# Kernel tuning notes

Hardware: AMD Instinct MI355X
Metric: run time of the kernel (lower is better)

## Reference

```python
import jax, jax.numpy as jnp
import numpy as np

EPS = 1e-5

def s_block(x, W, g, b, rm, rv):
    # Linear(no bias) -> BatchNorm1d (eval, running stats) -> 1 + tanh
    y = x @ W.T
    y = (y - rm) * jax.lax.rsqrt(rv + EPS) * g + b
    return 1.0 + jnp.tanh(y)

def si_block(x, cw, cb):
    # channel max/mean pool -> concat -> Conv2d(2,1,3,pad=1) -> sigmoid
    pooled = jnp.concatenate([x.max(axis=1, keepdims=True), x.mean(axis=1, keepdims=True)], axis=1)
    y = jax.lax.conv_general_dilated(pooled, cw, (1, 1), 'SAME',
                                     dimension_numbers=('NCHW', 'OIHW', 'NCHW'))
    return jax.nn.sigmoid(y + cb.reshape(1, 1, 1, 1))

def setup_inputs() -> dict:
    key = jax.random.key(0)
    ks = jax.random.split(key, 16)
    c = 640
    way, shot, batch, m = 5, 5, 4096, 25
    xav = (6.0 / (c + c)) ** 0.5  # xavier_uniform bound
    def lin(k):
        return jax.random.uniform(k, (c, c), jnp.float32, -xav, xav)
    def bn(k):
        k1, k2 = jax.random.split(k)
        return (1.0 + 0.1 * jax.random.normal(k1, (c,), jnp.float32),  # gamma
                0.1 * jax.random.normal(k2, (c,), jnp.float32),        # beta
                0.1 * jax.random.normal(jax.random.fold_in(k, 7), (c,), jnp.float32),  # running_mean
                jnp.ones((c,), jnp.float32))                           # running_var
    inp = {}
    inp['spt'] = jax.random.normal(ks[0], (way, shot, c, m), jnp.float32)
    inp['qry'] = jax.random.normal(ks[1], (batch, 1, c, m), jnp.float32)
    for i, name in enumerate(['p', 'q', 'prt', 'qry_s']):
        inp[f'W_{name}'] = lin(ks[2 + i])
        g, b, rm, rv = bn(ks[6 + i])
        inp[f'g_{name}'], inp[f'b_{name}'], inp[f'rm_{name}'], inp[f'rv_{name}'] = g, b, rm, rv
    inp['cw_p'] = 0.1 * jax.random.normal(ks[10], (1, 2, 3, 3), jnp.float32)
    inp['cb_p'] = jnp.zeros((1,), jnp.float32)
    inp['cw_q'] = 0.1 * jax.random.normal(ks[11], (1, 2, 3, 3), jnp.float32)
    inp['cb_q'] = jnp.zeros((1,), jnp.float32)
    return inp

def reference(spt, qry,
              W_p, g_p, b_p, rm_p, rv_p,
              W_q, g_q, b_q, rm_q, rv_q,
              W_prt, g_prt, b_prt, rm_prt, rv_prt,
              W_qry_s, g_qry_s, b_qry_s, rm_qry_s, rv_qry_s,
              cw_p, cb_p, cw_q, cb_q):
    way, shot, c, m = spt.shape
    batch = qry.shape[0]
    ws = way * shot
    prt = spt.reshape(ws, c, m)
    q_ = qry[:, 0]                                   # [batch, c, m]
    s = s_block(prt.mean(axis=-1), W_p, g_p, b_p, rm_p, rv_p)   # [ws, c]
    qg = s_block(q_.mean(axis=-1), W_q, g_q, b_q, rm_q, rv_q)   # [batch, c]
    prt = prt * s[:, :, None]
    q_ = q_ * qg[:, :, None]
    prt2 = si_block(prt.reshape(ws, c, 5, 5), cw_p, cb_p)       # [ws,1,5,5]
    qry2 = si_block(q_.reshape(batch, c, 5, 5), cw_q, cb_q)     # [batch,1,5,5]
    dist1 = jnp.sum((prt - prt2.reshape(ws, 1, m)) ** 2, axis=-1)    # [ws, c]
    dist2 = jnp.sum((q_ - qry2.reshape(batch, 1, m)) ** 2, axis=-1)  # [batch, c]
    w_prt = s_block(-dist1, W_prt, g_prt, b_prt, rm_prt, rv_prt)     # [ws, c]
    w_qry = s_block(-dist2, W_qry_s, g_qry_s, b_qry_s, rm_qry_s, rv_qry_s)  # [batch, c]
    # eval mode: add_noise is identity
    return 0.5 * w_prt[:, None, :] + 0.5 * w_qry[None, :, :]    # [ws, batch, c]
```

## Files before the change

### kernel.cpp

```cpp
#include <hip/hip_runtime.h>
#include <math.h>

#define CCH   640
#define MM    25
#define NB    4096
#define WSR   25
#define ROWF  16000
#define SLAB  (NB*CCH)

typedef float fx4 __attribute__((ext_vector_type(4)));
typedef short bf8 __attribute__((ext_vector_type(8)));
typedef float f32x4 __attribute__((ext_vector_type(4)));

static __device__ __forceinline__ void load4(float* dst, const float* p) {
  __builtin_memcpy(dst, p, 16);
}

static __device__ __forceinline__ unsigned short bf16_rne(float x) {
  unsigned u = __builtin_bit_cast(unsigned, x);
  return (unsigned short)((u + 0x7FFFu + ((u >> 16) & 1u)) >> 16);
}

__global__ __launch_bounds__(256) void rowmean_all_k(
    const float* __restrict__ spt, const float* __restrict__ qry,
    float* __restrict__ pmean, float* __restrict__ qmean, int n) {
  int idx = blockIdx.x * 256 + threadIdx.x;
  if (idx >= n) return;
  int row = idx / CCH, c = idx - row * CCH;
  const float* p;
  float* dst;
  if (row < WSR) { p = spt + (size_t)row * ROWF + c * MM; dst = pmean + idx; }
  else { p = qry + (size_t)(row - WSR) * ROWF + c * MM; dst = qmean + idx - WSR*CCH; }
  float s = 0.f;
  float v[4];
  #pragma unroll
  for (int j = 0; j < 6; ++j) {
    load4(v, p + 4*j);
    s += (v[0] + v[1]) + (v[2] + v[3]);
  }
  s += p[24];
  *dst = s * (1.f/25.f);
}

__global__ __launch_bounds__(256) void gemm2_k(
    const float* __restrict__ A0, const float* __restrict__ W0,
    const float* __restrict__ g0, const float* __restrict__ b0,
    const float* __restrict__ rm0, const float* __restrict__ rv0,
    int M0, float* __restrict__ out0,
    const float* __restrict__ A1, const float* __restrict__ W1,
    const float* __restrict__ g1, const float* __restrict__ b1,
    const float* __restrict__ rm1, const float* __restrict__ rv1,
    int M1, float* __restrict__ out1) {
  __shared__ short Ah[64*64], Al[64*64], Wh[64*64], Wl[64*64];
  const int bid = blockIdx.x;
  const float *A, *W, *gg, *bb, *rm, *rv;
  float* out;
  int M, i0, j0;
  if (bid < 10) {
    A = A0; W = W0; gg = g0; bb = b0; rm = rm0; rv = rv0; out = out0; M = M0;
    i0 = 0; j0 = bid * 64;
  } else {
    int b2 = bid - 10;
    A = A1; W = W1; gg = g1; bb = b1; rm = rm1; rv = rv1; out = out1; M = M1;
    i0 = (b2 / 10) * 64; j0 = (b2 % 10) * 64;
  }
  const int tid  = threadIdx.x;
  const int wave = tid >> 6, lane = tid & 63;
  const int lrow = lane & 15, lk = lane >> 4;

  f32x4 acc[4] = {{0.f,0.f,0.f,0.f},{0.f,0.f,0.f,0.f},
                  {0.f,0.f,0.f,0.f},{0.f,0.f,0.f,0.f}};

  const int srow0 = tid >> 3;
  const int sslot = tid & 7;

  for (int kt = 0; kt < CCH; kt += 64) {
    #pragma unroll
    for (int rnd = 0; rnd < 2; ++rnd) {
      int row  = srow0 + rnd * 32;
      int soff = row * 64 + ((sslot ^ (row & 7)) << 3);
      float a8[8];
      if (i0 + row < M) {
        const float* ap = A + (size_t)(i0 + row) * CCH + kt + sslot * 8;
        load4(a8, ap); load4(a8 + 4, ap + 4);
      } else {
        #pragma unroll
        for (int e = 0; e < 8; ++e) a8[e] = 0.f;
      }
      bf8 hv, lv;
      #pragma unroll
      for (int e = 0; e < 8; ++e) {
        unsigned short hb = bf16_rne(a8[e]);
        float hf = __builtin_bit_cast(float, (unsigned)hb << 16);
        hv[e] = (short)hb;
        lv[e] = (short)bf16_rne(a8[e] - hf);
      }
      *(bf8*)&Ah[soff] = hv;
      *(bf8*)&Al[soff] = lv;
      float w8[8];
      const float* wp_ = W + (size_t)(j0 + row) * CCH + kt + sslot * 8;
      load4(w8, wp_); load4(w8 + 4, wp_ + 4);
      #pragma unroll
      for (int e = 0; e < 8; ++e) {
        unsigned short hb = bf16_rne(w8[e]);
        float hf = __builtin_bit_cast(float, (unsigned)hb << 16);
        hv[e] = (short)hb;
        lv[e] = (short)bf16_rne(w8[e] - hf);
      }
      *(bf8*)&Wh[soff] = hv;
      *(bf8*)&Wl[soff] = lv;
    }
    __syncthreads();
    #pragma unroll
    for (int ks = 0; ks < 2; ++ks) {
      const int arow = wave * 16 + lrow;
      const int slot = ks * 4 + lk;
      const int aoff = arow * 64 + ((slot ^ (arow & 7)) << 3);
      bf8 afh = *(const bf8*)&Ah[aoff];
      bf8 afl = *(const bf8*)&Al[aoff];
      #pragma unroll
      for (int n = 0; n < 4; ++n) {
        const int wrow = n * 16 + lrow;
        const int woff = wrow * 64 + ((slot ^ (wrow & 7)) << 3);
        bf8 wfh = *(const bf8*)&Wh[woff];
        bf8 wfl = *(const bf8*)&Wl[woff];
        acc[n] = __builtin_amdgcn_mfma_f32_16x16x32_bf16(afh, wfh, acc[n], 0, 0, 0);
        acc[n] = __builtin_amdgcn_mfma_f32_16x16x32_bf16(afl, wfh, acc[n], 0, 0, 0);
        acc[n] = __builtin_amdgcn_mfma_f32_16x16x32_bf16(afh, wfl, acc[n], 0, 0, 0);
      }
    }
    __syncthreads();
  }
  #pragma unroll
  for (int n = 0; n < 4; ++n) {
    int j = j0 + n * 16 + lrow;
    float s  = rsqrtf(rv[j] + 1e-5f) * gg[j];
    float sh = bb[j] - rm[j] * s;
    #pragma unroll
    for (int r = 0; r < 4; ++r) {
      int row = i0 + wave * 16 + lk * 4 + r;
      if (row < M)
        out[(size_t)row * CCH + j] = 1.f + tanhf(fmaf(acc[n][r], s, sh));
    }
  }
}

__global__ __launch_bounds__(320, 4) void pcd_all_k(
    const float* __restrict__ spt, const float* __restrict__ qry,
    const float* __restrict__ sbuf, const float* __restrict__ qg,
    const float* __restrict__ cw_p, const float* __restrict__ cb_p,
    const float* __restrict__ cw_q, const float* __restrict__ cb_q,
    float* __restrict__ nd1, float* __restrict__ nd2) {
  const int blk = blockIdx.x;
  const int t = threadIdx.x;
  const float *row, *scl, *cw, *cbp;
  float* ndist;
  if (blk < WSR) {
    row = spt + (size_t)blk * ROWF; scl = sbuf + (size_t)blk * CCH;
    cw = cw_p; cbp = cb_p; ndist = nd1 + (size_t)blk * CCH;
  } else {
    int b = blk - WSR;
    row = qry + (size_t)b * ROWF; scl = qg + (size_t)b * CCH;
    cw = cw_q; cbp = cb_q; ndist = nd2 + (size_t)b * CCH;
  }
  __shared__ float xp[320 * MM];
  __shared__ float part[10][MM];
  __shared__ float pooled[2][MM];
  __shared__ float vbuf[MM];

  const float sc0 = scl[t];
  const float sc1 = scl[t + 320];

  float x0[MM], x1[MM];
  {
    const float* p0 = row + t * MM;
    const float* p1 = row + (t + 320) * MM;
    float v[4];
    #pragma unroll
    for (int j = 0; j < 6; ++j) {
      load4(v, p0 + 4*j);
      x0[4*j+0] = v[0]*sc0; x0[4*j+1] = v[1]*sc0; x0[4*j+2] = v[2]*sc0; x0[4*j+3] = v[3]*sc0;
    }
    x0[24] = p0[24] * sc0;
    #pragma unroll
    for (int j = 0; j < 6; ++j) {
      load4(v, p1 + 4*j);
      x1[4*j+0] = v[0]*sc1; x1[4*j+1] = v[1]*sc1; x1[4*j+2] = v[2]*sc1; x1[4*j+3] = v[3]*sc1;
    }
    x1[24] = p1[24] * sc1;
  }

  #pragma unroll
  for (int p = 0; p < MM; ++p) xp[t*MM + p] = fmaxf(x0[p], x1[p]);
  __syncthreads();
  if (t < 250) {
    int g = t / MM, p = t - g * MM;
    float m = -3.4e38f;
    #pragma unroll
    for (int k = 0; k < 32; ++k) m = fmaxf(m, xp[(g*32 + k)*MM + p]);
    part[g][p] = m;
  }
  __syncthreads();
  if (t < MM) {
    float m = -3.4e38f;
    #pragma unroll
    for (int g = 0; g < 10; ++g) m = fmaxf(m, part[g][t]);
    pooled[0][t] = m;
  }
  __syncthreads();
  #pragma unroll
  for (int p = 0; p < MM; ++p) xp[t*MM + p] = x0[p] + x1[p];
  __syncthreads();
  if (t < 250) {
    int g = t / MM, p = t - g * MM;
    float s = 0.f;
    #pragma unroll
    for (int k = 0; k < 32; ++k) s += xp[(g*32 + k)*MM + p];
    part[g][p] = s;
  }
  __syncthreads();
  if (t < MM) {
    float s = 0.f;
    #pragma unroll
    for (int g = 0; g < 10; ++g) s += part[g][t];
    pooled[1][t] = s * (1.f/640.f);
  }
  __syncthreads();
  if (t < MM) {
    int h = t / 5, w_ = t % 5;
    float y = cbp[0];
    #pragma unroll
    for (int ci = 0; ci < 2; ++ci)
      #pragma unroll
      for (int kh = 0; kh < 3; ++kh)
        #pragma unroll
        for (int kw = 0; kw < 3; ++kw) {
          int hh = h + kh - 1, ww = w_ + kw - 1;
          if (hh >= 0 && hh < 5 && ww >= 0 && ww < 5)
            y += pooled[ci][hh*5 + ww] * cw[ci*9 + kh*3 + kw];
        }
    vbuf[t] = 1.f / (1.f + expf(-y));
  }
  __syncthreads();
  float d0 = 0.f, d1 = 0.f;
  #pragma unroll
  for (int p = 0; p < MM; ++p) {
    float v = vbuf[p];
    float a = x0[p] - v; d0 = fmaf(a, a, d0);
    float e = x1[p] - v; d1 = fmaf(e, e, d1);
  }
  ndist[t]       = -d0;
  ndist[t + 320] = -d1;
}

__global__ __launch_bounds__(256) void combine_k(const float* __restrict__ wq,
    const float* __restrict__ wp, float* __restrict__ out) {
  const unsigned S4 = SLAB / 4;
  unsigned idx = blockIdx.x * 256 + threadIdx.x;
  unsigned w = idx / S4;
  unsigned rem = idx - w * S4;
  int c = (int)((rem * 4) % CCH);
  fx4 q = ((const fx4*)wq)[rem];
  fx4 p = *(const fx4*)(wp + w*CCH + c);
  fx4 o = 0.5f * (q + p);
  __builtin_nontemporal_store(o, (fx4*)out + idx);
}

__global__ __launch_bounds__(256) void combine24_k(const float* __restrict__ wq,
    const float* __restrict__ wp, float* __restrict__ out) {
  const size_t S4 = (size_t)SLAB / 4;
  size_t idx = (size_t)blockIdx.x * 256 + threadIdx.x;
  int slot = (int)(idx / S4);
  size_t rem = idx - (size_t)slot * S4;
  int w = (slot < 3) ? slot : slot + 1;
  int c = (int)((rem * 4) % CCH);
  float4 q = ((const float4*)wq)[rem];
  float4 p = *(const float4*)(wp + w*CCH + c);
  float4 o;
  o.x = 0.5f*(q.x + p.x); o.y = 0.5f*(q.y + p.y);
  o.z = 0.5f*(q.z + p.z); o.w = 0.5f*(q.w + p.w);
  ((float4*)out)[(size_t)w * S4 + rem] = o;
}

__global__ __launch_bounds__(256) void combine3_k(const float* __restrict__ wp,
                                                  float* __restrict__ out) {
  const size_t S4 = (size_t)SLAB / 4;
  size_t rem = (size_t)blockIdx.x * 256 + threadIdx.x;
  int c = (int)((rem * 4) % CCH);
  float4* ptr = (float4*)out + 3 * S4 + rem;
  float4 q = *ptr;
  float4 p = *(const float4*)(wp + 3*CCH + c);
  float4 o;
  o.x = 0.5f*(q.x + p.x); o.y = 0.5f*(q.y + p.y);
  o.z = 0.5f*(q.z + p.z); o.w = 0.5f*(q.w + p.w);
  *ptr = o;
}

extern "C" void kernel_launch(void* const* d_in, const int* in_sizes, int n_in,
                              void* d_out, int out_size, void* d_ws, size_t ws_size,
                              hipStream_t stream) {
  const float* spt    = (const float*)d_in[0];
  const float* qry    = (const float*)d_in[1];
  const float* W_p    = (const float*)d_in[2];
  const float* g_p    = (const float*)d_in[3];
  const float* b_p    = (const float*)d_in[4];
  const float* rm_p   = (const float*)d_in[5];
  const float* rv_p   = (const float*)d_in[6];
  const float* W_q    = (const float*)d_in[7];
  const float* g_q    = (const float*)d_in[8];
  const float* b_q    = (const float*)d_in[9];
  const float* rm_q   = (const float*)d_in[10];
  const float* rv_q   = (const float*)d_in[11];
  const float* W_prt  = (const float*)d_in[12];
  const float* g_prt  = (const float*)d_in[13];
  const float* b_prt  = (const float*)d_in[14];
  const float* rm_prt = (const float*)d_in[15];
  const float* rv_prt = (const float*)d_in[16];
  const float* W_qs   = (const float*)d_in[17];
  const float* g_qs   = (const float*)d_in[18];
  const float* b_qs   = (const float*)d_in[19];
  const float* rm_qs  = (const float*)d_in[20];
  const float* rv_qs  = (const float*)d_in[21];
  const float* cw_p   = (const float*)d_in[22];
  const float* cb_p   = (const float*)d_in[23];
  const float* cw_q   = (const float*)d_in[24];
  const float* cb_q   = (const float*)d_in[25];

  float* outp = (float*)d_out;
  float* ws   = (float*)d_ws;

  float* pmean  = ws;
  float* sbuf   = ws + 16000;
  float* ndist1 = ws + 32000;
  float* wprt   = ws + 48000;
  const size_t need = (size_t)(64000 + 3*SLAB) * sizeof(float);
  const bool big_ws = ws_size >= need;

  dim3 blk(256);
  dim3 blkp(320);
  const int nmean = (WSR + NB) * CCH;

  if (big_ws) {
    float* qmean  = ws + 64000;
    float* qg     = ws + 64000 + SLAB;
    float* ndist2 = ws + 64000 + 2*(size_t)SLAB;
    float* wqry   = qmean;
    rowmean_all_k<<<(nmean + 255)/256, blk, 0, stream>>>(spt, qry, pmean, qmean, nmean);
    gemm2_k<<<650, blk, 0, stream>>>(pmean, W_p, g_p, b_p, rm_p, rv_p, WSR, sbuf,
                                     qmean, W_q, g_q, b_q, rm_q, rv_q, NB, qg);
    pcd_all_k<<<WSR + NB, blkp, 0, stream>>>(spt, qry, sbuf, qg,
                                             cw_p, cb_p, cw_q, cb_q, ndist1, ndist2);
    gemm2_k<<<650, blk, 0, stream>>>(ndist1, W_prt, g_prt, b_prt, rm_prt, rv_prt, WSR, wprt,
                                     ndist2, W_qs, g_qs, b_qs, rm_qs, rv_qs, NB, wqry);
    combine_k<<<25 * (SLAB/4) / 256, blk, 0, stream>>>(wqry, wprt, outp);
  } else {
    float* qmean  = outp + 0 * (size_t)SLAB;
    float* qg     = outp + 1 * (size_t)SLAB;
    float* ndist2 = outp + 2 * (size_t)SLAB;
    float* wqry   = outp + 3 * (size_t)SLAB;
    rowmean_all_k<<<(nmean + 255)/256, blk, 0, stream>>>(spt, qry, pmean, qmean, nmean);
    gemm2_k<<<650, blk, 0, stream>>>(pmean, W_p, g_p, b_p, rm_p, rv_p, WSR, sbuf,
                                     qmean, W_q, g_q, b_q, rm_q, rv_q, NB, qg);
    pcd_all_k<<<WSR + NB, blkp, 0, stream>>>(spt, qry, sbuf, qg,
                                             cw_p, cb_p, cw_q, cb_q, ndist1, ndist2);
    gemm2_k<<<650, blk, 0, stream>>>(ndist1, W_prt, g_prt, b_prt, rm_prt, rv_prt, WSR, wprt,
                                     ndist2, W_qs, g_qs, b_qs, rm_qs, rv_qs, NB, wqry);
    combine24_k<<<(24 * (SLAB/4)) / 256, blk, 0, stream>>>(wqry, wprt, outp);
    combine3_k<<<(SLAB/4) / 256, blk, 0, stream>>>(wprt, outp);
  }
}
```

Before: 189.0 us.

## Pre-split GEMM operands into bf16 hi/lo once instead of per tile

Adds a prep kernel that computes row means and converts all four weight matrices into bf16 high/low pairs once. The pooled-distance kernel now writes its output directly as bf16 hi/lo. A new GEMM kernel loads these pre-split operands, which removes the repeated fp32-to-bf16 splitting that every block did for its A and W tiles. In exchange it needs a much larger workspace, the prep kernel adds extra writes and reads, and the four weight matrices are converted on every call.

```diff
diff --git a/kernel.cpp b/kernel.cpp
--- a/kernel.cpp
+++ b/kernel.cpp
@@ -7,18 +7,75 @@
 #define WSR   25
 #define ROWF  16000
 #define SLAB  (NB*CCH)
+#define WELEM (CCH*CCH)
+#define NMEAN ((WSR+NB)*CCH)
+#define NMEAN_B ((NMEAN + 255)/256)
+#define NW_B  (WELEM/256)
 
 typedef float fx4 __attribute__((ext_vector_type(4)));
 typedef short bf8 __attribute__((ext_vector_type(8)));
+typedef short s4  __attribute__((ext_vector_type(4)));
 typedef float f32x4 __attribute__((ext_vector_type(4)));
 
 static __device__ __forceinline__ void load4(float* dst, const float* p) {
   __builtin_memcpy(dst, p, 16);
 }
-
 static __device__ __forceinline__ unsigned short bf16_rne(float x) {
   unsigned u = __builtin_bit_cast(unsigned, x);
   return (unsigned short)((u + 0x7FFFu + ((u >> 16) & 1u)) >> 16);
+}
+static __device__ __forceinline__ float bfh2f(unsigned short h) {
+  return __builtin_bit_cast(float, (unsigned)h << 16);
+}
+
+__global__ __launch_bounds__(256) void prep_k(
+    const float* __restrict__ spt, const float* __restrict__ qry,
+    const float* __restrict__ W_p, const float* __restrict__ W_q,
+    const float* __restrict__ W_prt, const float* __restrict__ W_qs,
+    short* __restrict__ pmh, short* __restrict__ pml,
+    short* __restrict__ qmh, short* __restrict__ qml,
+    short* __restrict__ wph, short* __restrict__ wpl,
+    short* __restrict__ wqh, short* __restrict__ wql,
+    short* __restrict__ wrh, short* __restrict__ wrl,
+    short* __restrict__ wsh, short* __restrict__ wsl) {
+  const int bid = blockIdx.x;
+  if (bid < NMEAN_B) {
+    int idx = bid * 256 + threadIdx.x;
+    if (idx >= NMEAN) return;
+    int row = idx / CCH, c = idx - row * CCH;
+    const float* p;
+    short *dh, *dl; int off;
+    if (row < WSR) { p = spt + (size_t)row * ROWF + c * MM; dh = pmh; dl = pml; off = idx; }
+    else {
+      p = qry + (size_t)(row - WSR) * ROWF + c * MM;
+      dh = qmh; dl = qml; off = idx - WSR*CCH;
+    }
+    float s = 0.f, v[4];
+    #pragma unroll
+    for (int j = 0; j < 6; ++j) { load4(v, p + 4*j); s += (v[0]+v[1]) + (v[2]+v[3]); }
+    s += p[24];
+    s *= (1.f/25.f);
+    unsigned short hb = bf16_rne(s);
+    dh[off] = (short)hb;
+    dl[off] = (short)bf16_rne(s - bfh2f(hb));
+  } else {
+    int t = (bid - NMEAN_B) * 256 + threadIdx.x;
+    int mi = t / (WELEM/4);
+    int ei = (t - mi * (WELEM/4)) * 4;
+    const float* W = (mi==0) ? W_p : (mi==1) ? W_q : (mi==2) ? W_prt : W_qs;
+    short* dh = (mi==0) ? wph : (mi==1) ? wqh : (mi==2) ? wrh : wsh;
+    short* dl = (mi==0) ? wpl : (mi==1) ? wql : (mi==2) ? wrl : wsl;
+    fx4 v = *(const fx4*)(W + ei);
+    s4 h, l;
+    #pragma unroll
+    for (int e = 0; e < 4; ++e) {
+      unsigned short hb = bf16_rne(v[e]);
+      h[e] = (short)hb;
+      l[e] = (short)bf16_rne(v[e] - bfh2f(hb));
+    }
+    *(s4*)(dh + ei) = h;
+    *(s4*)(dl + ei) = l;
+  }
 }
 
 __global__ __launch_bounds__(256) void rowmean_all_k(
@@ -31,15 +88,98 @@
   float* dst;
   if (row < WSR) { p = spt + (size_t)row * ROWF + c * MM; dst = pmean + idx; }
   else { p = qry + (size_t)(row - WSR) * ROWF + c * MM; dst = qmean + idx - WSR*CCH; }
-  float s = 0.f;
-  float v[4];
+  float s = 0.f, v[4];
   #pragma unroll
-  for (int j = 0; j < 6; ++j) {
-    load4(v, p + 4*j);
-    s += (v[0] + v[1]) + (v[2] + v[3]);
-  }
+  for (int j = 0; j < 6; ++j) { load4(v, p + 4*j); s += (v[0]+v[1]) + (v[2]+v[3]); }
   s += p[24];
   *dst = s * (1.f/25.f);
+}
+
+__global__ __launch_bounds__(256) void gemm2_bf_k(
+    const short* __restrict__ Ah0, const short* __restrict__ Al0,
+    const short* __restrict__ Wh0, const short* __restrict__ Wl0,
+    const float* __restrict__ g0, const float* __restrict__ b0,
+    const float* __restrict__ rm0, const float* __restrict__ rv0,
+    int M0, float* __restrict__ out0,
+    const short* __restrict__ Ah1, const short* __restrict__ Al1,
+    const short* __restrict__ Wh1, const short* __restrict__ Wl1,
+    const float* __restrict__ g1, const float* __restrict__ b1,
+    const float* __restrict__ rm1, const float* __restrict__ rv1,
+    int M1, float* __restrict__ out1) {
+  __shared__ short sAh[64*64], sAl[64*64], sWh[64*64], sWl[64*64];
+  const int bid = blockIdx.x;
+  const short *Ah, *Al, *Wh, *Wl;
+  const float *gg, *bb, *rm, *rv;
+  float* out;
+  int M, i0, j0;
+  if (bid < 10) {
+    Ah=Ah0; Al=Al0; Wh=Wh0; Wl=Wl0; gg=g0; bb=b0; rm=rm0; rv=rv0; out=out0; M=M0;
+    i0 = 0; j0 = bid * 64;
+  } else {
+    int b2 = bid - 10;
+    Ah=Ah1; Al=Al1; Wh=Wh1; Wl=Wl1; gg=g1; bb=b1; rm=rm1; rv=rv1; out=out1; M=M1;
+    i0 = (b2 / 10) * 64; j0 = (b2 % 10) * 64;
+  }
+  const int tid  = threadIdx.x;
+  const int wave = tid >> 6, lane = tid & 63;
+  const int lrow = lane & 15, lk = lane >> 4;
+
+  f32x4 acc[4] = {{0.f,0.f,0.f,0.f},{0.f,0.f,0.f,0.f},
+                  {0.f,0.f,0.f,0.f},{0.f,0.f,0.f,0.f}};
+  const int srow0 = tid >> 3;
+  const int sslot = tid & 7;
+  const bf8 zv = {0,0,0,0,0,0,0,0};
+
+  for (int kt = 0; kt < CCH; kt += 64) {
+    #pragma unroll
+    for (int rnd = 0; rnd < 2; ++rnd) {
+      int row  = srow0 + rnd * 32;
+      int soff = row * 64 + ((sslot ^ (row & 7)) << 3);
+      bf8 vah = zv, val = zv;
+      if (i0 + row < M) {
+        vah = *(const bf8*)(Ah + (size_t)(i0 + row) * CCH + kt + sslot * 8);
+        val = *(const bf8*)(Al + (size_t)(i0 + row) * CCH + kt + sslot * 8);
+      }
+      bf8 vwh = *(const bf8*)(Wh + (size_t)(j0 + row) * CCH + kt + sslot * 8);
+      bf8 vwl = *(const bf8*)(Wl + (size_t)(j0 + row) * CCH + kt + sslot * 8);
+      *(bf8*)&sAh[soff] = vah;
+      *(bf8*)&sAl[soff] = val;
+      *(bf8*)&sWh[soff] = vwh;
+      *(bf8*)&sWl[soff] = vwl;
+    }
+    __syncthreads();
+    #pragma unroll
+    for (int ks = 0; ks < 2; ++ks) {
+      const int arow = wave * 16 + lrow;
+      const int slot = ks * 4 + lk;
+      const int aoff = arow * 64 + ((slot ^ (arow & 7)) << 3);
+      bf8 afh = *(const bf8*)&sAh[aoff];
+      bf8 afl = *(const bf8*)&sAl[aoff];
+      #pragma unroll
+      for (int n = 0; n < 4; ++n) {
+        const int wrow = n * 16 + lrow;
+        const int woff = wrow * 64 + ((slot ^ (wrow & 7)) << 3);
+        bf8 wfh = *(const bf8*)&sWh[woff];
+        bf8 wfl = *(const bf8*)&sWl[woff];
+        acc[n] = __builtin_amdgcn_mfma_f32_16x16x32_bf16(afh, wfh, acc[n], 0, 0, 0);
+        acc[n] = __builtin_amdgcn_mfma_f32_16x16x32_bf16(afl, wfh, acc[n], 0, 0, 0);
+        acc[n] = __builtin_amdgcn_mfma_f32_16x16x32_bf16(afh, wfl, acc[n], 0, 0, 0);
+      }
+    }
+    __syncthreads();
+  }
+  #pragma unroll
+  for (int n = 0; n < 4; ++n) {
+    int j = j0 + n * 16 + lrow;
+    float s  = rsqrtf(rv[j] + 1e-5f) * gg[j];
+    float sh = bb[j] - rm[j] * s;
+    #pragma unroll
+    for (int r = 0; r < 4; ++r) {
+      int row = i0 + wave * 16 + lk * 4 + r;
+      if (row < M)
+        out[(size_t)row * CCH + j] = 1.f + tanhf(fmaf(acc[n][r], s, sh));
+    }
+  }
 }
 
 __global__ __launch_bounds__(256) void gemm2_k(
@@ -67,13 +207,10 @@
   const int tid  = threadIdx.x;
   const int wave = tid >> 6, lane = tid & 63;
   const int lrow = lane & 15, lk = lane >> 4;
-
   f32x4 acc[4] = {{0.f,0.f,0.f,0.f},{0.f,0.f,0.f,0.f},
                   {0.f,0.f,0.f,0.f},{0.f,0.f,0.f,0.f}};
-
   const int srow0 = tid >> 3;
   const int sslot = tid & 7;
-
   for (int kt = 0; kt < CCH; kt += 64) {
     #pragma unroll
     for (int rnd = 0; rnd < 2; ++rnd) {
@@ -91,9 +228,8 @@
       #pragma unroll
       for (int e = 0; e < 8; ++e) {
         unsigned short hb = bf16_rne(a8[e]);
-        float hf = __builtin_bit_cast(float, (unsigned)hb << 16);
         hv[e] = (short)hb;
-        lv[e] = (short)bf16_rne(a8[e] - hf);
+        lv[e] = (short)bf16_rne(a8[e] - bfh2f(hb));
       }
       *(bf8*)&Ah[soff] = hv;
       *(bf8*)&Al[soff] = lv;
@@ -103,9 +239,8 @@
       #pragma unroll
       for (int e = 0; e < 8; ++e) {
         unsigned short hb = bf16_rne(w8[e]);
-        float hf = __builtin_bit_cast(float, (unsigned)hb << 16);
         hv[e] = (short)hb;
-        lv[e] = (short)bf16_rne(w8[e] - hf);
+        lv[e] = (short)bf16_rne(w8[e] - bfh2f(hb));
       }
       *(bf8*)&Wh[soff] = hv;
       *(bf8*)&Wl[soff] = lv;
@@ -145,23 +280,30 @@
   }
 }
 
+template<bool BF>
 __global__ __launch_bounds__(320, 4) void pcd_all_k(
     const float* __restrict__ spt, const float* __restrict__ qry,
     const float* __restrict__ sbuf, const float* __restrict__ qg,
     const float* __restrict__ cw_p, const float* __restrict__ cb_p,
     const float* __restrict__ cw_q, const float* __restrict__ cb_q,
-    float* __restrict__ nd1, float* __restrict__ nd2) {
+    float* __restrict__ nd1f, float* __restrict__ nd2f,
+    short* __restrict__ nd1h, short* __restrict__ nd1l,
+    short* __restrict__ nd2h, short* __restrict__ nd2l) {
   const int blk = blockIdx.x;
   const int t = threadIdx.x;
   const float *row, *scl, *cw, *cbp;
-  float* ndist;
+  float* ndf; short *ndh, *ndl;
   if (blk < WSR) {
     row = spt + (size_t)blk * ROWF; scl = sbuf + (size_t)blk * CCH;
-    cw = cw_p; cbp = cb_p; ndist = nd1 + (size_t)blk * CCH;
+    cw = cw_p; cbp = cb_p;
+    ndf = nd1f ? nd1f + (size_t)blk * CCH : nullptr;
+    ndh = nd1h + (size_t)blk * CCH; ndl = nd1l + (size_t)blk * CCH;
   } else {
     int b = blk - WSR;
     row = qry + (size_t)b * ROWF; scl = qg + (size_t)b * CCH;
-    cw = cw_q; cbp = cb_q; ndist = nd2 + (size_t)b * CCH;
+    cw = cw_q; cbp = cb_q;
+    ndf = nd2f ? nd2f + (size_t)b * CCH : nullptr;
+    ndh = nd2h + (size_t)b * CCH; ndl = nd2l + (size_t)b * CCH;
   }
   __shared__ float xp[320 * MM];
   __shared__ float part[10][MM];
@@ -249,8 +391,17 @@
     float a = x0[p] - v; d0 = fmaf(a, a, d0);
     float e = x1[p] - v; d1 = fmaf(e, e, d1);
   }
-  ndist[t]       = -d0;
-  ndist[t + 320] = -d1;
+  if (BF) {
+    float n0 = -d0, n1 = -d1;
+    unsigned short h0 = bf16_rne(n0), h1 = bf16_rne(n1);
+    ndh[t]       = (short)h0;
+    ndl[t]       = (short)bf16_rne(n0 - bfh2f(h0));
+    ndh[t + 320] = (short)h1;
+    ndl[t + 320] = (short)bf16_rne(n1 - bfh2f(h1));
+  } else {
+    ndf[t]       = -d0;
+    ndf[t + 320] = -d1;
+  }
 }
 
 __global__ __launch_bounds__(256) void combine_k(const float* __restrict__ wq,
@@ -329,40 +480,59 @@
   float* outp = (float*)d_out;
   float* ws   = (float*)d_ws;
 
-  float* pmean  = ws;
-  float* sbuf   = ws + 16000;
-  float* ndist1 = ws + 32000;
-  float* wprt   = ws + 48000;
-  const size_t need = (size_t)(64000 + 3*SLAB) * sizeof(float);
-  const bool big_ws = ws_size >= need;
-
   dim3 blk(256);
   dim3 blkp(320);
-  const int nmean = (WSR + NB) * CCH;
+
+  const size_t fl_count = 32000 + 2*(size_t)SLAB;
+  const size_t sh_count = 4*16000 + 4*(size_t)SLAB + 8*(size_t)WELEM;
+  const size_t need = fl_count*sizeof(float) + sh_count*sizeof(short);
+  const bool big_ws = ws_size >= need;
 
   if (big_ws) {
-    float* qmean  = ws + 64000;
-    float* qg     = ws + 64000 + SLAB;
-    float* ndist2 = ws + 64000 + 2*(size_t)SLAB;
-    float* wqry   = qmean;
-    rowmean_all_k<<<(nmean + 255)/256, blk, 0, stream>>>(spt, qry, pmean, qmean, nmean);
-    gemm2_k<<<650, blk, 0, stream>>>(pmean, W_p, g_p, b_p, rm_p, rv_p, WSR, sbuf,
-                                     qmean, W_q, g_q, b_q, rm_q, rv_q, NB, qg);
-    pcd_all_k<<<WSR + NB, blkp, 0, stream>>>(spt, qry, sbuf, qg,
-                                             cw_p, cb_p, cw_q, cb_q, ndist1, ndist2);
-    gemm2_k<<<650, blk, 0, stream>>>(ndist1, W_prt, g_prt, b_prt, rm_prt, rv_prt, WSR, wprt,
-                                     ndist2, W_qs, g_qs, b_qs, rm_qs, rv_qs, NB, wqry);
+    float* sbuf = ws;
+    float* wprt = ws + 16000;
+    float* qg   = ws + 32000;
+    float* wqry = ws + 32000 + (size_t)SLAB;
+    short* sp   = (short*)(ws + fl_count);
+    short* pmh  = sp;            short* pml  = sp + 16000;
+    short* nd1h = sp + 32000;    short* nd1l = sp + 48000;
+    short* qmh  = sp + 64000;
+    short* qml  = qmh + (size_t)SLAB;
+    short* nd2h = qml + (size_t)SLAB;
+    short* nd2l = nd2h + (size_t)SLAB;
+    short* wph  = nd2l + (size_t)SLAB;
+    short* wpl  = wph + WELEM;
+    short* wqh  = wpl + WELEM;  short* wql = wqh + WELEM;
+    short* wrh  = wql + WELEM;  short* wrl = wrh + WELEM;
+    short* wsh  = wrl + WELEM;  short* wsl = wsh + WELEM;
+
+    prep_k<<<NMEAN_B + NW_B, blk, 0, stream>>>(spt, qry, W_p, W_q, W_prt, W_qs,
+        pmh, pml, qmh, qml, wph, wpl, wqh, wql, wrh, wrl, wsh, wsl);
+    gemm2_bf_k<<<650, blk, 0, stream>>>(
+        pmh, pml, wph, wpl, g_p, b_p, rm_p, rv_p, WSR, sbuf,
+        qmh, qml, wqh, wql, g_q, b_q, rm_q, rv_q, NB, qg);
+    pcd_all_k<true><<<WSR + NB, blkp, 0, stream>>>(spt, qry, sbuf, qg,
+        cw_p, cb_p, cw_q, cb_q, nullptr, nullptr, nd1h, nd1l, nd2h, nd2l);
+    gemm2_bf_k<<<650, blk, 0, stream>>>(
+        nd1h, nd1l, wrh, wrl, g_prt, b_prt, rm_prt, rv_prt, WSR, wprt,
+        nd2h, nd2l, wsh, wsl, g_qs, b_qs, rm_qs, rv_qs, NB, wqry);
     combine_k<<<25 * (SLAB/4) / 256, blk, 0, stream>>>(wqry, wprt, outp);
   } else {
+    float* pmean  = ws;
+    float* sbuf   = ws + 16000;
+    float* ndist1 = ws + 32000;
+    float* wprt   = ws + 48000;
     float* qmean  = outp + 0 * (size_t)SLAB;
     float* qg     = outp + 1 * (size_t)SLAB;
     float* ndist2 = outp + 2 * (size_t)SLAB;
     float* wqry   = outp + 3 * (size_t)SLAB;
+    const int nmean = (WSR + NB) * CCH;
     rowmean_all_k<<<(nmean + 255)/256, blk, 0, stream>>>(spt, qry, pmean, qmean, nmean);
     gemm2_k<<<650, blk, 0, stream>>>(pmean, W_p, g_p, b_p, rm_p, rv_p, WSR, sbuf,
                                      qmean, W_q, g_q, b_q, rm_q, rv_q, NB, qg);
-    pcd_all_k<<<WSR + NB, blkp, 0, stream>>>(spt, qry, sbuf, qg,
-                                             cw_p, cb_p, cw_q, cb_q, ndist1, ndist2);
+    pcd_all_k<false><<<WSR + NB, blkp, 0, stream>>>(spt, qry, sbuf, qg,
+        cw_p, cb_p, cw_q, cb_q, ndist1, ndist2,
+        (short*)ws, (short*)ws, (short*)ws, (short*)ws);
     gemm2_k<<<650, blk, 0, stream>>>(ndist1, W_prt, g_prt, b_prt, rm_prt, rv_prt, WSR, wprt,
                                      ndist2, W_qs, g_qs, b_qs, rm_qs, rv_qs, NB, wqry);
     combine24_k<<<(24 * (SLAB/4)) / 256, blk, 0, stream>>>(wqry, wprt, outp);
```

Result: no change. 186.4 us (-1.4%).
